# Kernel optimization log

Hardware: AMD Instinct MI355X
Metric: run time of the kernel (lower is better)

## Reference

```python
import jax, jax.numpy as jnp
import numpy as np

NUM_USERS = 100000
NUM_ITEMS = 50000
EMBED = 64
S_NNZ = NUM_USERS * 32   # avg social degree 32
R_NNZ = NUM_USERS * 50   # avg 50 rated items per user
BATCH = 8192


def setup_inputs() -> dict:
    key = jax.random.key(0)
    ks = jax.random.split(key, 12)
    d = EMBED
    # Embedding tables (xavier-uniform style scale)
    U = jax.random.uniform(ks[0], (NUM_USERS, d), jnp.float32, -1.0, 1.0) * np.sqrt(6.0 / (NUM_USERS + d))
    V = jax.random.uniform(ks[1], (NUM_ITEMS, d), jnp.float32, -1.0, 1.0) * np.sqrt(6.0 / (NUM_ITEMS + d))
    # Diffusion layer weights: Linear(2d -> d). Stored as [2d, d] (x @ W + b).
    lim = np.sqrt(6.0 / (3 * d))
    W0 = jax.random.uniform(ks[2], (2 * d, d), jnp.float32, -lim, lim)
    b0 = jnp.zeros((d,), jnp.float32)
    W1 = jax.random.uniform(ks[3], (2 * d, d), jnp.float32, -lim, lim)
    b1 = jnp.zeros((d,), jnp.float32)
    # Sparse social matrix S [NUM_USERS, NUM_USERS], COO edge lists, row-normalized values.
    S_row = jax.random.randint(ks[4], (S_NNZ,), 0, NUM_USERS, jnp.int32)
    S_col = jax.random.randint(ks[5], (S_NNZ,), 0, NUM_USERS, jnp.int32)
    S_val = jnp.full((S_NNZ,), 1.0 / 32.0, jnp.float32)
    # Sparse rating matrix R [NUM_USERS, NUM_ITEMS]
    R_row = jax.random.randint(ks[6], (R_NNZ,), 0, NUM_USERS, jnp.int32)
    R_col = jax.random.randint(ks[7], (R_NNZ,), 0, NUM_ITEMS, jnp.int32)
    R_val = jnp.full((R_NNZ,), 1.0 / 50.0, jnp.float32)
    batch_user = jax.random.randint(ks[8], (BATCH,), 0, NUM_USERS, jnp.int64 if jax.config.jax_enable_x64 else jnp.int32)
    batch_pos_item = jax.random.randint(ks[9], (BATCH,), 0, NUM_ITEMS, jnp.int32)
    batch_neg_item = jax.random.randint(ks[10], (BATCH,), 0, NUM_ITEMS, jnp.int32)
    return dict(batch_user=batch_user, batch_pos_item=batch_pos_item, batch_neg_item=batch_neg_item,
                U=U, V=V, W0=W0, b0=b0, W1=W1, b1=b1,
                S_row=S_row, S_col=S_col, S_val=S_val,
                R_row=R_row, R_col=R_col, R_val=R_val)


def _spmm(row, col, val, X, n_rows):
    # (sparse [n_rows, n] COO) @ X : gather + scale + segment-sum
    return jax.ops.segment_sum(val[:, None] * X[col], row, num_segments=n_rows)


def reference(batch_user, batch_pos_item, batch_neg_item, U, V, W0, b0, W1, b1,
              S_row, S_col, S_val, R_row, R_col, R_val):
    # Diffusion layers: U <- relu(concat([S @ U, U]) @ W + b)
    for W, b in ((W0, b0), (W1, b1)):
        agg = _spmm(S_row, S_col, S_val, U, NUM_USERS)          # [num_users, d]
        U = jax.nn.relu(jnp.concatenate([agg, U], axis=1) @ W + b)
    user_g = U + _spmm(R_row, R_col, R_val, V, NUM_USERS)        # [num_users, d]
    bu = user_g[batch_user]          # [B, d]
    bp = V[batch_pos_item]           # [B, d]
    bn = V[batch_neg_item]           # [B, d]
    return (bu, bp, bn)
```

## Files before the change

kernel.cpp:

```cpp
#include <hip/hip_runtime.h>
#include <hip/hip_bf16.h>

#define NUM_USERS 100000
#define NUM_ITEMS 50000
#define EMBED     64
#define S_NNZ     (NUM_USERS * 32)
#define R_NNZ     (NUM_USERS * 50)
#define BATCH     8192

#define NB    256
#define NCH   256
#define CHUNK (S_NNZ / NCH)
#define BROWS 391


__global__ __launch_bounds__(256) void k_p1hist(const int* __restrict__ rows, int* __restrict__ cnt_t) {
    __shared__ int h[NB];
    int t = threadIdx.x, b = blockIdx.x;
    h[t] = 0;
    __syncthreads();
    int base = b * CHUNK;
    for (int i = t; i < CHUNK; i += 256) atomicAdd(&h[rows[base + i] / BROWS], 1);
    __syncthreads();
    cnt_t[t * NCH + b] = h[t];
}

__global__ __launch_bounds__(1024) void k_scan1(const int* __restrict__ cnt, int* __restrict__ excl,
                                                int* __restrict__ bsums, int n) {
    __shared__ int buf[1024];
    int t = threadIdx.x;
    int i = blockIdx.x * 1024 + t;
    int x = (i < n) ? cnt[i] : 0;
    buf[t] = x;
    __syncthreads();
    for (int off = 1; off < 1024; off <<= 1) {
        int y = (t >= off) ? buf[t - off] : 0;
        __syncthreads();
        buf[t] += y;
        __syncthreads();
    }
    if (i < n) excl[i] = buf[t] - x;
    if (t == 1023) bsums[blockIdx.x] = buf[1023];
}

__global__ __launch_bounds__(1024) void k_scan2(int* __restrict__ bsums, int nb, int* __restrict__ total_slot) {
    __shared__ int buf[1024];
    int t = threadIdx.x;
    int x = (t < nb) ? bsums[t] : 0;
    buf[t] = x;
    __syncthreads();
    for (int off = 1; off < 1024; off <<= 1) {
        int y = (t >= off) ? buf[t - off] : 0;
        __syncthreads();
        buf[t] += y;
        __syncthreads();
    }
    if (t < nb) bsums[t] = buf[t] - x;
    if (t == 1023) total_slot[0] = buf[1023];
}

__global__ void k_scan3b(int* __restrict__ a, const int* __restrict__ bsums, int n) {
    int i = blockIdx.x * blockDim.x + threadIdx.x;
    if (i < n) a[i] += bsums[i >> 10];
}

__global__ __launch_bounds__(256) void k_p1scatter(const int* __restrict__ rows, const int* __restrict__ cols,
                                                   const float* __restrict__ vals, const int* __restrict__ cnt_t,
                                                   int2* __restrict__ tmpE) {
    __shared__ int cur[NB];
    int t = threadIdx.x, b = blockIdx.x;
    cur[t] = cnt_t[t * NCH + b];
    __syncthreads();
    int base = b * CHUNK;
    for (int i = t; i < CHUNK; i += 256) {
        int e  = base + i;
        int r  = rows[e];
        int bk = r / BROWS;
        int pos = atomicAdd(&cur[bk], 1);
        tmpE[pos] = make_int2(((r - bk * BROWS) << 17) | cols[e], __float_as_int(vals[e]));
    }
}

__global__ __launch_bounds__(512) void k_p2(const int2* __restrict__ tmpE, const int* __restrict__ cnt_t,
                                            int* __restrict__ rowptr, int2* __restrict__ colval) {
    __shared__ int h[512];
    __shared__ int s[512];
    __shared__ int cur[512];
    int t = threadIdx.x, k = blockIdx.x;
    int beg = cnt_t[k * NCH];
    int end = (k < NB - 1) ? cnt_t[(k + 1) * NCH] : S_NNZ;
    h[t] = 0;
    __syncthreads();
    for (int j = beg + t; j < end; j += 512) atomicAdd(&h[((unsigned)tmpE[j].x) >> 17], 1);
    __syncthreads();
    s[t] = h[t];
    __syncthreads();
    for (int off = 1; off < 512; off <<= 1) {
        int y = (t >= off) ? s[t - off] : 0;
        __syncthreads();
        s[t] += y;
        __syncthreads();
    }
    int excl = s[t] - h[t];
    int gr   = k * BROWS + t;
    if (t <= BROWS && gr <= NUM_USERS) rowptr[gr] = beg + excl;
    cur[t] = beg + excl;
    __syncthreads();
    for (int j = beg + t; j < end; j += 512) {
        int2 e  = tmpE[j];
        int pos = atomicAdd(&cur[((unsigned)e.x) >> 17], 1);
        colval[pos] = make_int2(e.x & 0x1FFFF, e.y);
    }
}

__global__ void k_cvt(const float* __restrict__ src, __hip_bfloat16* __restrict__ dst, int n) {
    int i = blockIdx.x * blockDim.x + threadIdx.x;
    if (i < n) dst[i] = __float2bfloat16(src[i]);
}

__global__ __launch_bounds__(256) void k_spmm16(const int* __restrict__ rowptr,
                                                const int2* __restrict__ colval,
                                                const __hip_bfloat16* __restrict__ X,
                                                float* __restrict__ Y, int n_rows) {
    int w    = blockIdx.x * (blockDim.x >> 6) + (threadIdx.x >> 6);
    int lane = threadIdx.x & 63;
    if (w >= n_rows) return;
    int beg = rowptr[w], end = rowptr[w + 1];
    float acc = 0.0f;
    int j    = beg;
    int jend = beg + ((end - beg) & ~7);
    for (; j < jend; j += 8) {
        int2 cv[8];
#pragma unroll
        for (int u = 0; u < 8; ++u) cv[u] = colval[j + u];
        float x[8];
#pragma unroll
        for (int u = 0; u < 8; ++u) x[u] = __bfloat162float(X[(size_t)cv[u].x * EMBED + lane]);
#pragma unroll
        for (int u = 0; u < 8; ++u) acc = fmaf(__int_as_float(cv[u].y), x[u], acc);
    }
    for (; j < end; ++j)
        acc = fmaf(__int_as_float(colval[j].y), __bfloat162float(X[(size_t)colval[j].x * EMBED + lane]), acc);
    Y[(size_t)w * EMBED + lane] = acc;
}

__global__ __launch_bounds__(256) void k_spmm_batch16(const int* __restrict__ rowptr,
                                                      const int2* __restrict__ colval,
                                                      const __hip_bfloat16* __restrict__ X,
                                                      const int* __restrict__ bu,
                                                      float* __restrict__ Agg2, int n) {
    int w    = blockIdx.x * (blockDim.x >> 6) + (threadIdx.x >> 6);
    int lane = threadIdx.x & 63;
    if (w >= n) return;
    int r   = bu[w];
    int beg = rowptr[r], end = rowptr[r + 1];
    float acc = 0.0f;
    int j    = beg;
    int jend = beg + ((end - beg) & ~7);
    for (; j < jend; j += 8) {
        int2 cv[8];
#pragma unroll
        for (int u = 0; u < 8; ++u) cv[u] = colval[j + u];
        float x[8];
#pragma unroll
        for (int u = 0; u < 8; ++u) x[u] = __bfloat162float(X[(size_t)cv[u].x * EMBED + lane]);
#pragma unroll
        for (int u = 0; u < 8; ++u) acc = fmaf(__int_as_float(cv[u].y), x[u], acc);
    }
    for (; j < end; ++j)
        acc = fmaf(__int_as_float(colval[j].y), __bfloat162float(X[(size_t)colval[j].x * EMBED + lane]), acc);
    Agg2[(size_t)w * EMBED + lane] = acc;
}

__global__ __launch_bounds__(256) void k_layer(const float* __restrict__ Agg,
                                               const float* __restrict__ Uin,
                                               float* __restrict__ Uout,
                                               __hip_bfloat16* __restrict__ Uout16,
                                               const float* __restrict__ W,
                                               const float* __restrict__ b) {
    __shared__ float Wl[128 * 64];
    __shared__ float xs[16][128];
    int t = threadIdx.x;
    for (int i = t; i < 128 * 64; i += 256) Wl[i] = W[i];
    int rl = t >> 6;
    int c  = t & 63;
    int rbase = blockIdx.x * 16;
#pragma unroll
    for (int q = 0; q < 4; ++q) {
        int rr = rbase + rl * 4 + q;
        if (rr < NUM_USERS) {
            xs[rl * 4 + q][c]      = Agg[(size_t)rr * EMBED + c];
            xs[rl * 4 + q][64 + c] = Uin[(size_t)rr * EMBED + c];
        }
    }
    __syncthreads();
    float bias = b[c];
#pragma unroll
    for (int q = 0; q < 4; ++q) {
        int rr = rbase + rl * 4 + q;
        if (rr >= NUM_USERS) break;
        float acc = bias;
#pragma unroll
        for (int k = 0; k < 128; ++k) acc = fmaf(xs[rl * 4 + q][k], Wl[k * 64 + c], acc);
        float v = fmaxf(acc, 0.0f);
        Uout[(size_t)rr * EMBED + c]   = v;
        Uout16[(size_t)rr * EMBED + c] = __float2bfloat16(v);
    }
}

__global__ __launch_bounds__(256) void k_layer_batch(const float* __restrict__ Agg2,
                                                     const float* __restrict__ Uin,
                                                     const int* __restrict__ bu,
                                                     float* __restrict__ out0,
                                                     const float* __restrict__ W,
                                                     const float* __restrict__ b) {
    __shared__ float Wl[128 * 64];
    __shared__ float xs[16][128];
    int t = threadIdx.x;
    for (int i = t; i < 128 * 64; i += 256) Wl[i] = W[i];
    int rl = t >> 6;
    int c  = t & 63;
    int rbase = blockIdx.x * 16;
#pragma unroll
    for (int q = 0; q < 4; ++q) {
        int s = rbase + rl * 4 + q;
        if (s < BATCH) {
            xs[rl * 4 + q][c]      = Agg2[(size_t)s * EMBED + c];
            xs[rl * 4 + q][64 + c] = Uin[(size_t)bu[s] * EMBED + c];
        }
    }
    __syncthreads();
    float bias = b[c];
#pragma unroll
    for (int q = 0; q < 4; ++q) {
        int s = rbase + rl * 4 + q;
        if (s >= BATCH) break;
        float acc = bias;
#pragma unroll
        for (int k = 0; k < 128; ++k) acc = fmaf(xs[rl * 4 + q][k], Wl[k * 64 + c], acc);
        out0[(size_t)s * EMBED + c] = fmaxf(acc, 0.0f);
    }
}


__global__ void k_chain(const int* __restrict__ bu, int* __restrict__ head,
                        int* __restrict__ nxt, int n) {
    int i = blockIdx.x * blockDim.x + threadIdx.x;
    if (i < n) nxt[i] = atomicExch(&head[bu[i]], i);
}

__global__ __launch_bounds__(256) void k_filter16(const int* __restrict__ rows,
                                                  const int* __restrict__ cols,
                                                  const float* __restrict__ vals,
                                                  const int* __restrict__ head,
                                                  const int* __restrict__ nxt,
                                                  const __hip_bfloat16* __restrict__ V16,
                                                  float* __restrict__ out0, int nnz) {
    int e    = blockIdx.x * blockDim.x + threadIdx.x;
    int lane = threadIdx.x & 63;
    int r = (e < nnz) ? rows[e] : -1;
    int h = (r >= 0) ? head[r] : -1;
    unsigned long long mask = __ballot(h >= 0);
    int   c = 0;
    float v = 0.0f;
    if (h >= 0) { c = cols[e]; v = vals[e]; }
    while (mask) {
        int l = __ffsll((long long)mask) - 1;
        mask &= mask - 1;
        int   cc = __shfl(c, l);
        float vv = __shfl(v, l);
        int   hh = __shfl(h, l);
        float x  = vv * __bfloat162float(V16[(size_t)cc * EMBED + lane]);
        while (hh >= 0) {
            atomicAdd(&out0[(size_t)hh * EMBED + lane], x);
            hh = nxt[hh];
        }
    }
}

__global__ void k_gather2(const float* __restrict__ V,
                          const int* __restrict__ bp, const int* __restrict__ bn,
                          float* __restrict__ out) {
    int i = blockIdx.x * blockDim.x + threadIdx.x;
    if (i >= BATCH * EMBED) return;
    int row = i >> 6, l = i & 63;
    out[BATCH * EMBED + i]     = V[(size_t)bp[row] * EMBED + l];
    out[2 * BATCH * EMBED + i] = V[(size_t)bn[row] * EMBED + l];
}


extern "C" void kernel_launch(void* const* d_in, const int* in_sizes, int n_in,
                              void* d_out, int out_size, void* d_ws, size_t ws_size,
                              hipStream_t stream) {
    const int*   batch_user = (const int*)d_in[0];
    const int*   batch_pos  = (const int*)d_in[1];
    const int*   batch_neg  = (const int*)d_in[2];
    const float* U     = (const float*)d_in[3];
    const float* V     = (const float*)d_in[4];
    const float* W0    = (const float*)d_in[5];
    const float* b0    = (const float*)d_in[6];
    const float* W1    = (const float*)d_in[7];
    const float* b1    = (const float*)d_in[8];
    const int*   S_row = (const int*)d_in[9];
    const int*   S_col = (const int*)d_in[10];
    const float* S_val = (const float*)d_in[11];
    const int*   R_row = (const int*)d_in[12];
    const int*   R_col = (const int*)d_in[13];
    const float* R_val = (const float*)d_in[14];
    float* out = (float*)d_out;

    const size_t tabElems = (size_t)NUM_USERS * EMBED;

    char* wsb = (char*)d_ws;
    size_t o = 0;
    float* A       = (float*)(wsb + o); o += tabElems * 4;
    float* B       = (float*)(wsb + o); o += tabElems * 4;
    float* Agg2    = (float*)(wsb + o); o += (size_t)BATCH * EMBED * 4;
    int*   rowptrS = (int*)(wsb + o);   o += (NUM_USERS + 1) * 4;
    int*   cnt_t   = (int*)(wsb + o);   o += (size_t)NB * NCH * 4;
    int*   bsums   = (int*)(wsb + o);   o += 1024 * 4;
    int*   head    = (int*)(wsb + o);   o += NUM_USERS * 4;
    int*   nxt     = (int*)(wsb + o);   o += BATCH * 4;
    o = (o + 7) & ~(size_t)7;
    int2*  colvalS = (int2*)(wsb + o);  o += (size_t)S_NNZ * 8;
    __hip_bfloat16* X16 = (__hip_bfloat16*)(wsb + o); o += tabElems * 2;

    int2* tmpE = (int2*)A;

    const int spmm_blocks  = (NUM_USERS * 64 + 255) / 256;
    const int layer_blocks = (NUM_USERS + 15) / 16;

    k_p1hist<<<NCH, 256, 0, stream>>>(S_row, cnt_t);
    k_scan1<<<(NB * NCH) / 1024, 1024, 0, stream>>>(cnt_t, cnt_t, bsums, NB * NCH);
    k_scan2<<<1, 1024, 0, stream>>>(bsums, (NB * NCH) / 1024, &bsums[512]);
    k_scan3b<<<(NB * NCH) / 256, 256, 0, stream>>>(cnt_t, bsums, NB * NCH);
    k_p1scatter<<<NCH, 256, 0, stream>>>(S_row, S_col, S_val, cnt_t, tmpE);
    k_p2<<<NB, 512, 0, stream>>>(tmpE, cnt_t, rowptrS, colvalS);

    k_cvt<<<(int)((tabElems + 255) / 256), 256, 0, stream>>>(U, X16, (int)tabElems);
    k_spmm16<<<spmm_blocks, 256, 0, stream>>>(rowptrS, colvalS, X16, B, NUM_USERS);
    k_layer<<<layer_blocks, 256, 0, stream>>>(B, U, A, X16, W0, b0);

    hipMemsetAsync(head, 0xFF, NUM_USERS * sizeof(int), stream);
    k_chain<<<(BATCH + 255) / 256, 256, 0, stream>>>(batch_user, head, nxt, BATCH);

    k_spmm_batch16<<<(BATCH * 64 + 255) / 256, 256, 0, stream>>>(rowptrS, colvalS, X16, batch_user, Agg2, BATCH);
    k_layer_batch<<<(BATCH + 15) / 16, 256, 0, stream>>>(Agg2, A, batch_user, out, W1, b1);

    k_cvt<<<(int)(((size_t)NUM_ITEMS * EMBED + 255) / 256), 256, 0, stream>>>(V, X16, NUM_ITEMS * EMBED);
    k_filter16<<<(R_NNZ + 255) / 256, 256, 0, stream>>>(R_row, R_col, R_val, head, nxt, X16, out, R_NNZ);

    k_gather2<<<(BATCH * EMBED + 255) / 256, 256, 0, stream>>>(V, batch_pos, batch_neg, out);
}
```

Baseline: 598.9 us.

## Replace atomic R-filter scatter with compacted CSR build and per-user SpMM

Instead of scanning all rating edges and atomically adding bf16-converted V rows into the batch outputs for each matching edge, the code counts matching edges per batch slot, scans the counts, scatters column/value pairs into a compact CSR, then runs a wave-per-user gather-accumulate with no float atomics. This removes many float atomics on output rows and turns them into register accumulation. In exchange it adds three passes over R_row (count, scatter) plus a single-block scan, and uses integer atomics on slot counters.

```diff
diff --git a/kernel.cpp b/kernel.cpp
--- a/kernel.cpp
+++ b/kernel.cpp
@@ -249,32 +249,87 @@
     if (i < n) nxt[i] = atomicExch(&head[bu[i]], i);
 }
 
-__global__ __launch_bounds__(256) void k_filter16(const int* __restrict__ rows,
+__global__ __launch_bounds__(256) void k_rcount(const int* __restrict__ rows,
+                                                const int* __restrict__ head,
+                                                int* __restrict__ cnt, int nnz) {
+    int e = blockIdx.x * blockDim.x + threadIdx.x;
+    if (e >= nnz) return;
+    int h = head[rows[e]];
+    if (h >= 0) atomicAdd(&cnt[h], 1);
+}
+
+__global__ __launch_bounds__(1024) void k_rscan(const int* __restrict__ cnt,
+                                                int* __restrict__ rowptr2,
+                                                int* __restrict__ cur) {
+    __shared__ int buf[1024];
+    int t = threadIdx.x;
+    int loc[8];
+    int sum = 0;
+#pragma unroll
+    for (int q = 0; q < 8; ++q) { loc[q] = cnt[t * 8 + q]; sum += loc[q]; }
+    buf[t] = sum;
+    __syncthreads();
+    for (int off = 1; off < 1024; off <<= 1) {
+        int y = (t >= off) ? buf[t - off] : 0;
+        __syncthreads();
+        buf[t] += y;
+        __syncthreads();
+    }
+    int excl = buf[t] - sum;
+#pragma unroll
+    for (int q = 0; q < 8; ++q) {
+        rowptr2[t * 8 + q] = excl;
+        cur[t * 8 + q]     = excl;
+        excl += loc[q];
+    }
+    if (t == 1023) rowptr2[BATCH] = excl;
+}
+
+__global__ __launch_bounds__(256) void k_rscatter(const int* __restrict__ rows,
                                                   const int* __restrict__ cols,
                                                   const float* __restrict__ vals,
                                                   const int* __restrict__ head,
-                                                  const int* __restrict__ nxt,
-                                                  const __hip_bfloat16* __restrict__ V16,
-                                                  float* __restrict__ out0, int nnz) {
-    int e    = blockIdx.x * blockDim.x + threadIdx.x;
+                                                  int* __restrict__ cur,
+                                                  int2* __restrict__ colval2, int nnz) {
+    int e = blockIdx.x * blockDim.x + threadIdx.x;
+    if (e >= nnz) return;
+    int h = head[rows[e]];
+    if (h < 0) return;
+    int pos = atomicAdd(&cur[h], 1);
+    colval2[pos] = make_int2(cols[e], __float_as_int(vals[e]));
+}
+
+__global__ __launch_bounds__(256) void k_rspmm(const int* __restrict__ rowptr2,
+                                               const int2* __restrict__ colval2,
+                                               const __hip_bfloat16* __restrict__ V16,
+                                               const int* __restrict__ bu,
+                                               const int* __restrict__ head,
+                                               const int* __restrict__ nxt,
+                                               float* __restrict__ out0) {
+    int s    = blockIdx.x * (blockDim.x >> 6) + (threadIdx.x >> 6);
     int lane = threadIdx.x & 63;
-    int r = (e < nnz) ? rows[e] : -1;
-    int h = (r >= 0) ? head[r] : -1;
-    unsigned long long mask = __ballot(h >= 0);
-    int   c = 0;
-    float v = 0.0f;
-    if (h >= 0) { c = cols[e]; v = vals[e]; }
-    while (mask) {
-        int l = __ffsll((long long)mask) - 1;
-        mask &= mask - 1;
-        int   cc = __shfl(c, l);
-        float vv = __shfl(v, l);
-        int   hh = __shfl(h, l);
-        float x  = vv * __bfloat162float(V16[(size_t)cc * EMBED + lane]);
-        while (hh >= 0) {
-            atomicAdd(&out0[(size_t)hh * EMBED + lane], x);
-            hh = nxt[hh];
-        }
+    if (s >= BATCH) return;
+    if (head[bu[s]] != s) return;
+    int beg = rowptr2[s], end = rowptr2[s + 1];
+    float acc = 0.0f;
+    int j    = beg;
+    int jend = beg + ((end - beg) & ~7);
+    for (; j < jend; j += 8) {
+        int2 cv[8];
+#pragma unroll
+        for (int u = 0; u < 8; ++u) cv[u] = colval2[j + u];
+        float x[8];
+#pragma unroll
+        for (int u = 0; u < 8; ++u) x[u] = __bfloat162float(V16[(size_t)cv[u].x * EMBED + lane]);
+#pragma unroll
+        for (int u = 0; u < 8; ++u) acc = fmaf(__int_as_float(cv[u].y), x[u], acc);
+    }
+    for (; j < end; ++j)
+        acc = fmaf(__int_as_float(colval2[j].y), __bfloat162float(V16[(size_t)colval2[j].x * EMBED + lane]), acc);
+    int slot = s;
+    while (slot >= 0) {
+        out0[(size_t)slot * EMBED + lane] += acc;
+        slot = nxt[slot];
     }
 }
 
@@ -321,11 +376,15 @@
     int*   bsums   = (int*)(wsb + o);   o += 1024 * 4;
     int*   head    = (int*)(wsb + o);   o += NUM_USERS * 4;
     int*   nxt     = (int*)(wsb + o);   o += BATCH * 4;
+    int*   cntR    = (int*)(wsb + o);   o += BATCH * 4;
+    int*   rowptr2 = (int*)(wsb + o);   o += (BATCH + 1) * 4;
+    int*   curR    = (int*)(wsb + o);   o += BATCH * 4;
     o = (o + 7) & ~(size_t)7;
     int2*  colvalS = (int2*)(wsb + o);  o += (size_t)S_NNZ * 8;
     __hip_bfloat16* X16 = (__hip_bfloat16*)(wsb + o); o += tabElems * 2;
 
-    int2* tmpE = (int2*)A;
+    int2* tmpE    = (int2*)A;
+    int2* colval2 = (int2*)A;
 
     const int spmm_blocks  = (NUM_USERS * 64 + 255) / 256;
     const int layer_blocks = (NUM_USERS + 15) / 16;
@@ -347,8 +406,12 @@
     k_spmm_batch16<<<(BATCH * 64 + 255) / 256, 256, 0, stream>>>(rowptrS, colvalS, X16, batch_user, Agg2, BATCH);
     k_layer_batch<<<(BATCH + 15) / 16, 256, 0, stream>>>(Agg2, A, batch_user, out, W1, b1);
 
+    hipMemsetAsync(cntR, 0, BATCH * sizeof(int), stream);
+    k_rcount<<<(R_NNZ + 255) / 256, 256, 0, stream>>>(R_row, head, cntR, R_NNZ);
+    k_rscan<<<1, 1024, 0, stream>>>(cntR, rowptr2, curR);
+    k_rscatter<<<(R_NNZ + 255) / 256, 256, 0, stream>>>(R_row, R_col, R_val, head, curR, colval2, R_NNZ);
     k_cvt<<<(int)(((size_t)NUM_ITEMS * EMBED + 255) / 256), 256, 0, stream>>>(V, X16, NUM_ITEMS * EMBED);
-    k_filter16<<<(R_NNZ + 255) / 256, 256, 0, stream>>>(R_row, R_col, R_val, head, nxt, X16, out, R_NNZ);
+    k_rspmm<<<(BATCH * 64 + 255) / 256, 256, 0, stream>>>(rowptr2, colval2, X16, batch_user, head, nxt, out);
 
     k_gather2<<<(BATCH * EMBED + 255) / 256, 256, 0, stream>>>(V, batch_pos, batch_neg, out);
 }
```

Result: no change. 606.5 us (+1.3%).
